# Performance work log

Hardware: AMD Instinct MI355X
Metric: run time of the kernel (lower is better)

Reference implementation:

```python
import jax, jax.numpy as jnp
import numpy as np

HIDDEN = 512
NHEADS = 8
ALPHA = 0.1
NUM_HOP = 4
MASK_VAL = -16384.0
LN_EPS = 1e-5


def setup_inputs() -> dict:
    key = jax.random.key(0)
    ks = jax.random.split(key, 10)
    B, N, H = 8, 1024, HIDDEN
    s = 1.0 / np.sqrt(H)
    x = jax.random.normal(ks[0], (B, N, H), dtype=jnp.float32)
    adj = jax.random.randint(ks[1], (B, N, N), 0, 2, dtype=jnp.int32)
    Wq = jax.random.uniform(ks[2], (H, H), jnp.float32, -s, s)
    bq = jax.random.uniform(ks[3], (H,), jnp.float32, -s, s)
    Wk = jax.random.uniform(ks[4], (H, H), jnp.float32, -s, s)
    bk = jax.random.uniform(ks[5], (H,), jnp.float32, -s, s)
    Wv = jax.random.uniform(ks[6], (H, H), jnp.float32, -s, s)
    bv = jax.random.uniform(ks[7], (H,), jnp.float32, -s, s)
    gamma = jnp.ones((H,), jnp.float32)
    beta = jnp.zeros((H,), jnp.float32)
    return {"x": x, "adj": adj, "Wq": Wq, "bq": bq, "Wk": Wk, "bk": bk,
            "Wv": Wv, "bv": bv, "gamma": gamma, "beta": beta}


def reference(x, adj, Wq, bq, Wk, bk, Wv, bv, gamma, beta):
    B, N, H = x.shape
    u = H // NHEADS
    # torch Linear: y = x @ W^T + b
    q = x @ Wq.T + bq  # [B,N,H]
    k = x @ Wk.T + bk
    v = x @ Wv.T + bv
    # split hidden into contiguous head chunks (matches per-head slicing)
    qh = q.reshape(B, N, NHEADS, u).transpose(0, 2, 1, 3)  # [B,Hd,N,u]
    kh = k.reshape(B, N, NHEADS, u).transpose(0, 2, 1, 3)
    vh = v.reshape(B, N, NHEADS, u).transpose(0, 2, 1, 3)
    scores = jnp.einsum('bhnd,bhmd->bhnm', qh, kh)  # [B,Hd,N,N]
    mask = (adj == 0)[:, None, :, :]  # broadcast over heads
    scores = jnp.where(mask, MASK_VAL, scores)
    pros = jax.nn.softmax(scores, axis=-1)
    z_init = vh
    z = z_init
    for _ in range(NUM_HOP):
        z = (1.0 - ALPHA) * jnp.einsum('bhnm,bhmd->bhnd', pros, z) + ALPHA * z_init
    h_prime = z.transpose(0, 2, 1, 3).reshape(B, N, H)  # concat heads
    y = x + h_prime
    mu = jnp.mean(y, axis=-1, keepdims=True)
    var = jnp.mean((y - mu) ** 2, axis=-1, keepdims=True)
    return (y - mu) / jnp.sqrt(var + LN_EPS) * gamma + beta
```

## Files before the change

kernel.cpp:

```cpp
#include <hip/hip_runtime.h>
#include <hip/hip_bf16.h>

#define BB 8
#define NN 1024
#define HH 512
#define NHEADS 8
#define UU 64

typedef __attribute__((ext_vector_type(8))) short short8;
typedef __attribute__((ext_vector_type(4))) float f32x4;
typedef unsigned short u16;
typedef unsigned char u8;

__device__ inline float b2f(unsigned short u) {
    union { float f; unsigned int i; } c; c.i = ((unsigned int)u) << 16; return c.f;
}
__device__ inline unsigned short f2b(float f) {
    __hip_bfloat16 h = __float2bfloat16(f);
    return *reinterpret_cast<unsigned short*>(&h);
}
__device__ inline void gl_lds16(const void* g, void* l) {
    __builtin_amdgcn_global_load_lds(
        (const __attribute__((address_space(1))) unsigned int*)g,
        (__attribute__((address_space(3))) unsigned int*)l, 16, 0, 0);
}

__global__ __launch_bounds__(256) void cvt_bf16(
    const float* __restrict__ x, const float* __restrict__ Wq,
    const float* __restrict__ Wk, const float* __restrict__ Wv,
    u16* __restrict__ xb, u16* __restrict__ Wb)
{
    const int which = blockIdx.y;
    const float* src;
    u16* dst;
    int n;
    if (which == 0) { src = x;  dst = xb;              n = BB * NN * HH; }
    else if (which == 1) { src = Wq; dst = Wb;             n = HH * HH; }
    else if (which == 2) { src = Wk; dst = Wb + HH * HH;   n = HH * HH; }
    else              { src = Wv; dst = Wb + 2 * HH * HH;  n = HH * HH; }

    const int base = (blockIdx.x * 256 + threadIdx.x) * 8;
    if (base >= n) return;
    const float4* sp = (const float4*)&src[base];
    float4 a = sp[0], b = sp[1];
    short8 o;
    o[0] = (short)f2b(a.x); o[1] = (short)f2b(a.y);
    o[2] = (short)f2b(a.z); o[3] = (short)f2b(a.w);
    o[4] = (short)f2b(b.x); o[5] = (short)f2b(b.y);
    o[6] = (short)f2b(b.z); o[7] = (short)f2b(b.w);
    *(short8*)&dst[base] = o;
}

__global__ __launch_bounds__(256) void adj_pack(
    const int* __restrict__ adj, unsigned int* __restrict__ adjp)
{
    const int wave = threadIdx.x >> 6, lane = threadIdx.x & 63;
    const int row = blockIdx.x * 4 + wave;
    const int* ar = adj + (size_t)row * NN;
    unsigned long long* out = (unsigned long long*)(adjp + (size_t)row * 32);
    #pragma unroll
    for (int it = 0; it < 16; ++it) {
        int a = ar[it * 64 + lane];
        unsigned long long m = __ballot(a != 0);
        if (lane == 0) out[it] = m;
    }
}

__global__ __launch_bounds__(256) void qkv_gemm(
    const u16* __restrict__ xb, const u16* __restrict__ Wb,
    const float* __restrict__ bq, const float* __restrict__ bk,
    const float* __restrict__ bv,
    u16* __restrict__ q, u16* __restrict__ k, u16* __restrict__ v)
{
    const int which = blockIdx.z;
    const u16* W      = Wb + which * HH * HH;
    const float* bias = which == 0 ? bq : (which == 1 ? bk : bv);
    u16* out          = which == 0 ? q  : (which == 1 ? k  : v);

    const int tid = threadIdx.x;
    const int wave = tid >> 6, lane = tid & 63;
    const int ln = lane & 15, quad = lane >> 4;
    const int wr = (wave >> 1) * 64, wc = (wave & 1) * 64;
    const int rowbase = blockIdx.x * 128, colbase = blockIdx.y * 128;

    __shared__ __align__(16) u16 As[128 * 32];
    __shared__ __align__(16) u16 Bs[128 * 32];
    __shared__ __align__(16) u16 Cs[128 * 136];

    f32x4 acc[4][4];
    #pragma unroll
    for (int ri = 0; ri < 4; ++ri)
        #pragma unroll
        for (int ci = 0; ci < 4; ++ci) acc[ri][ci] = (f32x4){0.f, 0.f, 0.f, 0.f};

    const int lr = lane >> 2;
    const int lk = (lane & 3) * 8;

    for (int kk = 0; kk < HH; kk += 32) {
        __syncthreads();
        #pragma unroll
        for (int i = 0; i < 2; ++i) {
            int r = wave * 32 + i * 16 + lr;
            gl_lds16(&xb[(size_t)(rowbase + r) * HH + kk + lk],
                     (char*)As + (wave * 32 + i * 16) * 64);
            gl_lds16(&W[(size_t)(colbase + r) * HH + kk + lk],
                     (char*)Bs + (wave * 32 + i * 16) * 64);
        }
        __syncthreads();

        short8 bfr[4];
        #pragma unroll
        for (int ci = 0; ci < 4; ++ci)
            bfr[ci] = *(const short8*)&Bs[(wc + ci * 16 + ln) * 32 + quad * 8];
        #pragma unroll
        for (int ri = 0; ri < 4; ++ri) {
            short8 af = *(const short8*)&As[(wr + ri * 16 + ln) * 32 + quad * 8];
            #pragma unroll
            for (int ci = 0; ci < 4; ++ci)
                acc[ri][ci] = __builtin_amdgcn_mfma_f32_16x16x32_bf16(af, bfr[ci], acc[ri][ci], 0, 0, 0);
        }
    }

    #pragma unroll
    for (int ci = 0; ci < 4; ++ci) {
        int col = wc + ci * 16 + ln;
        float bb = bias[colbase + col];
        #pragma unroll
        for (int ri = 0; ri < 4; ++ri) {
            #pragma unroll
            for (int r = 0; r < 4; ++r) {
                int row = wr + ri * 16 + quad * 4 + r;
                Cs[row * 136 + col] = f2b(acc[ri][ci][r] + bb);
            }
        }
    }
    __syncthreads();
    {
        int row = tid >> 1, half = tid & 1;
        int gcol0 = colbase + half * 64;
        int hh = gcol0 >> 6;
        int grow = rowbase + row;
        int bidx = grow >> 10, n = grow & 1023;
        u16* op = &out[(((size_t)(bidx * NHEADS + hh)) * NN + n) * UU];
        const u16* cp = &Cs[row * 136 + half * 64];
        #pragma unroll
        for (int j = 0; j < 8; ++j)
            *(short8*)(op + j * 8) = *(const short8*)(cp + j * 8);
    }
}

__global__ __launch_bounds__(256) void vt8(
    const u16* __restrict__ v, u8* __restrict__ v8t)
{
    const int bh = blockIdx.x;
    const int t = threadIdx.x;
    const size_t hd = (size_t)bh << 16;
    __shared__ u16 tile[64][72];

    for (int chunk = 0; chunk < 16; ++chunk) {
        const int n0 = chunk * 64;
        const int r = t >> 2, cs = t & 3;
        const u16* vp = &v[((size_t)bh * NN + n0 + r) * UU + cs * 16];
        short8 a = *(const short8*)vp;
        short8 b8 = *(const short8*)(vp + 8);
        #pragma unroll
        for (int j = 0; j < 8; ++j) {
            tile[r][cs * 16 + j] = (u16)a[j];
            tile[r][cs * 16 + 8 + j] = (u16)b8[j];
        }
        __syncthreads();
        const int c = t & 63, qt = t >> 6;
        unsigned int w[4];
        #pragma unroll
        for (int g = 0; g < 4; ++g) {
            float f0 = b2f(tile[qt * 16 + g * 4 + 0][c]);
            float f1 = b2f(tile[qt * 16 + g * 4 + 1][c]);
            float f2 = b2f(tile[qt * 16 + g * 4 + 2][c]);
            float f3 = b2f(tile[qt * 16 + g * 4 + 3][c]);
            int lo = __builtin_amdgcn_cvt_pk_fp8_f32(f0, f1, 0, false);
            w[g] = (unsigned int)__builtin_amdgcn_cvt_pk_fp8_f32(f2, f3, lo, true);
        }
        uint4 o; o.x = w[0]; o.y = w[1]; o.z = w[2]; o.w = w[3];
        *(uint4*)&v8t[hd + (size_t)c * 1024 + n0 + qt * 16] = o;
        __syncthreads();
    }
}

__global__ __launch_bounds__(256, 4) void scores_softmax(
    const u16* __restrict__ q, const u16* __restrict__ kmat,
    const unsigned int* __restrict__ adjp, u8* __restrict__ P8)
{
    const int b = blockIdx.z, h = blockIdx.y, rt = blockIdx.x;
    const int bh = b * NHEADS + h;
    const int wave = threadIdx.x >> 6, lane = threadIdx.x & 63;
    const int ln = lane & 15, quad = lane >> 4;
    const int rowbase = rt * 16;

    __shared__ float redsum[4][16];
    __shared__ float scl[16];
    __shared__ __align__(16) u16 ebuf[16 * 1040];

    const u16* qp = &q[((size_t)bh * NN + rowbase + ln) * UU + quad * 8];
    short8 a0 = *(const short8*)qp;
    short8 a1 = *(const short8*)(qp + 32);

    float rsum[4] = {0.f, 0.f, 0.f, 0.f};

    #pragma unroll
    for (int hf = 0; hf < 2; ++hf) {
        unsigned int ab[4][4];
        #pragma unroll
        for (int r = 0; r < 4; ++r) {
            int row = rowbase + quad * 4 + r;
            *(uint4*)&ab[r][0] =
                *(const uint4*)&adjp[((size_t)(b * NN + row)) * 32 + wave * 8 + hf * 4];
        }

        f32x4 accs[8];
        #pragma unroll
        for (int ct = 0; ct < 8; ++ct) {
            int col = wave * 256 + hf * 128 + ct * 16 + ln;
            const u16* kp = &kmat[((size_t)bh * NN + col) * UU + quad * 8];
            short8 b0 = *(const short8*)kp;
            short8 b1 = *(const short8*)(kp + 32);
            f32x4 acc = (f32x4){0.f, 0.f, 0.f, 0.f};
            acc = __builtin_amdgcn_mfma_f32_16x16x32_bf16(a0, b0, acc, 0, 0, 0);
            acc = __builtin_amdgcn_mfma_f32_16x16x32_bf16(a1, b1, acc, 0, 0, 0);
            accs[ct] = acc;
        }

        #pragma unroll
        for (int ct = 0; ct < 8; ++ct) {
            const int dw = ct >> 1;
            const int bitpos = (ct & 1) * 16 + ln;
            const int col = wave * 256 + hf * 128 + ct * 16 + ln;
            #pragma unroll
            for (int r = 0; r < 4; ++r) {
                unsigned int on = (ab[r][dw] >> bitpos) & 1u;
                float e = on ? __expf(accs[ct][r] - 32.0f) : 0.0f;
                rsum[r] += e;
                ebuf[(quad * 4 + r) * 1040 + col] = f2b(e);
            }
        }
    }

    #pragma unroll
    for (int r = 0; r < 4; ++r) {
        #pragma unroll
        for (int off = 8; off >= 1; off >>= 1)
            rsum[r] += __shfl_xor(rsum[r], off);
    }
    if (ln == 0) {
        #pragma unroll
        for (int r = 0; r < 4; ++r) redsum[wave][quad * 4 + r] = rsum[r];
    }
    __syncthreads();
    if (wave == 0 && ln == 0) {
        #pragma unroll
        for (int r = 0; r < 4; ++r) {
            int row16 = quad * 4 + r;
            float s = redsum[0][row16] + redsum[1][row16]
                    + redsum[2][row16] + redsum[3][row16];
            scl[row16] = 16.0f / s;
        }
    }
    __syncthreads();

    u8* Pb = P8 + ((size_t)bh << 20) + rt * 16384;
    int cc = threadIdx.x * 2;
    #pragma unroll
    for (int i = 0; i < 2; ++i, ++cc) {
        const int kc = cc >> 4, r = cc & 15;
        const float s = scl[r];
        const u16* ep = &ebuf[r * 1040 + kc * 32];
        unsigned int w[8];
        #pragma unroll
        for (int g = 0; g < 8; ++g) {
            float f0 = b2f(ep[g * 4 + 0]) * s;
            float f1 = b2f(ep[g * 4 + 1]) * s;
            float f2 = b2f(ep[g * 4 + 2]) * s;
            float f3 = b2f(ep[g * 4 + 3]) * s;
            int lo = __builtin_amdgcn_cvt_pk_fp8_f32(f0, f1, 0, false);
            w[g] = (unsigned int)__builtin_amdgcn_cvt_pk_fp8_f32(f2, f3, lo, true);
        }
        uint4 o0; o0.x = w[0]; o0.y = w[1]; o0.z = w[2]; o0.w = w[3];
        uint4 o1; o1.x = w[4]; o1.y = w[5]; o1.z = w[6]; o1.w = w[7];
        *(uint4*)(Pb + cc * 32)      = o0;
        *(uint4*)(Pb + cc * 32 + 16) = o1;
    }
}

__global__ __launch_bounds__(512) void hop(
    const u8* __restrict__ P8, const u8* __restrict__ z8in,
    const u16* __restrict__ v, u8* __restrict__ z8out,
    u16* __restrict__ zbf_out, int last)
{
    const int b = blockIdx.z, h = blockIdx.y, rt = blockIdx.x;
    const int bh = b * NHEADS + h;
    const int tid = threadIdx.x;
    const int wave = tid >> 6, lane = tid & 63;
    const int ln = lane & 15, quad = lane >> 4;
    const int wrow = rt * 128 + wave * 16;

    __shared__ __align__(16) u8 zt[64 * 1040];

    const u8* zg = z8in + ((size_t)bh << 16);
    #pragma unroll
    for (int i = 0; i < 8; ++i) {
        int c = wave * 8 + i;
        gl_lds16(zg + (size_t)c * 1024 + lane * 16, (char*)zt + c * 1040);
    }
    __syncthreads();

    f32x4 acc[4];
    #pragma unroll
    for (int ci = 0; ci < 4; ++ci) acc[ci] = (f32x4){0.f, 0.f, 0.f, 0.f};

    const u8* pt = P8 + ((size_t)bh << 20) + (size_t)(rt * 8 + wave) * 16384
                 + ln * 32 + quad * 8;
    #pragma unroll 4
    for (int kc = 0; kc < 32; ++kc) {
        long a = *(const long*)(pt + kc * 512);
        int kk = kc * 32;
        #pragma unroll
        for (int ci = 0; ci < 4; ++ci) {
            long bz = *(const long*)&zt[(ci * 16 + ln) * 1040 + kk + quad * 8];
            acc[ci] = __builtin_amdgcn_mfma_f32_16x16x32_fp8_fp8(a, bz, acc[ci], 0, 0, 0);
        }
    }

    if (last) {
        #pragma unroll
        for (int ci = 0; ci < 4; ++ci) {
            int col = ci * 16 + ln;
            #pragma unroll
            for (int r = 0; r < 4; ++r) {
                int row = wrow + quad * 4 + r;
                float vv = b2f(v[((size_t)bh * NN + row) * UU + col]);
                zbf_out[((size_t)(b * NN + row)) * HH + h * UU + col]
                    = f2b(0.05625f * acc[ci][r] + 0.1f * vv);
            }
        }
    } else {
        u8* zo = z8out + ((size_t)bh << 16);
        #pragma unroll
        for (int ci = 0; ci < 4; ++ci) {
            int col = ci * 16 + ln;
            float zv[4];
            #pragma unroll
            for (int r = 0; r < 4; ++r) {
                int row = wrow + quad * 4 + r;
                float vv = b2f(v[((size_t)bh * NN + row) * UU + col]);
                zv[r] = 0.05625f * acc[ci][r] + 0.1f * vv;
            }
            int lo = __builtin_amdgcn_cvt_pk_fp8_f32(zv[0], zv[1], 0, false);
            unsigned int dw = (unsigned int)__builtin_amdgcn_cvt_pk_fp8_f32(zv[2], zv[3], lo, true);
            *(unsigned int*)&zo[(size_t)col * 1024 + wrow + quad * 4] = dw;
        }
    }
}

__global__ __launch_bounds__(256) void resid_ln(
    const float* __restrict__ x, const u16* __restrict__ z,
    const float* __restrict__ gamma, const float* __restrict__ beta,
    float* __restrict__ out)
{
    const int r = blockIdx.x * 4 + (threadIdx.x >> 6);
    const int lane = threadIdx.x & 63;
    const size_t base = (size_t)r * HH + lane * 8;

    const float4* xp = (const float4*)&x[base];
    float4 x0 = xp[0], x1 = xp[1];
    short8 zv = *(const short8*)&z[base];
    float y[8];
    y[0] = x0.x + b2f((u16)zv[0]); y[1] = x0.y + b2f((u16)zv[1]);
    y[2] = x0.z + b2f((u16)zv[2]); y[3] = x0.w + b2f((u16)zv[3]);
    y[4] = x1.x + b2f((u16)zv[4]); y[5] = x1.y + b2f((u16)zv[5]);
    y[6] = x1.z + b2f((u16)zv[6]); y[7] = x1.w + b2f((u16)zv[7]);

    float s = 0.f, sq = 0.f;
    #pragma unroll
    for (int j = 0; j < 8; ++j) { s += y[j]; sq += y[j] * y[j]; }
    #pragma unroll
    for (int off = 32; off >= 1; off >>= 1) {
        s  += __shfl_xor(s, off);
        sq += __shfl_xor(sq, off);
    }
    const float mu = s * (1.0f / HH);
    const float var = sq * (1.0f / HH) - mu * mu;
    const float rstd = rsqrtf(var + 1e-5f);

    const float4* gp = (const float4*)&gamma[lane * 8];
    const float4* bp = (const float4*)&beta[lane * 8];
    float4 g0 = gp[0], g1 = gp[1], b0 = bp[0], b1 = bp[1];

    float4 o0, o1;
    o0.x = (y[0] - mu) * rstd * g0.x + b0.x;
    o0.y = (y[1] - mu) * rstd * g0.y + b0.y;
    o0.z = (y[2] - mu) * rstd * g0.z + b0.z;
    o0.w = (y[3] - mu) * rstd * g0.w + b0.w;
    o1.x = (y[4] - mu) * rstd * g1.x + b1.x;
    o1.y = (y[5] - mu) * rstd * g1.y + b1.y;
    o1.z = (y[6] - mu) * rstd * g1.z + b1.z;
    o1.w = (y[7] - mu) * rstd * g1.w + b1.w;
    float4* op = (float4*)&out[base];
    op[0] = o0; op[1] = o1;
}

extern "C" void kernel_launch(void* const* d_in, const int* in_sizes, int n_in,
                              void* d_out, int out_size, void* d_ws, size_t ws_size,
                              hipStream_t stream)
{
    const float* x   = (const float*)d_in[0];
    const int* adj   = (const int*)d_in[1];
    const float* Wq  = (const float*)d_in[2];
    const float* bq  = (const float*)d_in[3];
    const float* Wk  = (const float*)d_in[4];
    const float* bk  = (const float*)d_in[5];
    const float* Wv  = (const float*)d_in[6];
    const float* bv  = (const float*)d_in[7];
    const float* gamma = (const float*)d_in[8];
    const float* beta  = (const float*)d_in[9];
    float* out = (float*)d_out;

    const size_t E = (size_t)BB * NN * HH;
    u16* ws16 = (u16*)d_ws;
    u16* xb = ws16;
    u16* q  = ws16 + E;
    u16* k  = ws16 + 2 * E;
    u16* v  = ws16 + 3 * E;
    u16* za = ws16 + 4 * E;
    u16* Wb = ws16 + 5 * E;
    u8* base8 = (u8*)(ws16 + 5 * E + 786432);
    u8* P8  = base8;
    u8* z8a = base8 + ((size_t)64 << 20);
    u8* z8b = z8a + ((size_t)4 << 20);
    u8* v8t = z8b + ((size_t)4 << 20);
    unsigned int* adjp = (unsigned int*)(v8t + ((size_t)4 << 20));

    cvt_bf16<<<dim3(2048, 4), 256, 0, stream>>>(x, Wq, Wk, Wv, xb, Wb);
    adj_pack<<<dim3(2048), 256, 0, stream>>>(adj, adjp);
    qkv_gemm<<<dim3(64, 4, 3), 256, 0, stream>>>(xb, Wb, bq, bk, bv, q, k, v);
    vt8<<<dim3(64), 256, 0, stream>>>(v, v8t);
    scores_softmax<<<dim3(64, NHEADS, BB), 256, 0, stream>>>(q, k, adjp, P8);
    hop<<<dim3(8, NHEADS, BB), 512, 0, stream>>>(P8, v8t, v, z8a, za, 0);
    hop<<<dim3(8, NHEADS, BB), 512, 0, stream>>>(P8, z8a, v, z8b, za, 0);
    hop<<<dim3(8, NHEADS, BB), 512, 0, stream>>>(P8, z8b, v, z8a, za, 0);
    hop<<<dim3(8, NHEADS, BB), 512, 0, stream>>>(P8, z8a, v, z8b, za, 1);
    resid_ln<<<dim3(2048), 256, 0, stream>>>(x, za, gamma, beta, out);
}
```

Baseline: 312.1 us.

## Fuse x bf16 conversion into QKV GEMM, split vt8, restructure scores softmax

The QKV GEMM now reads fp32 x directly and converts it to bf16 while staging into padded LDS, so the separate full-activation conversion pass and its intermediate buffer go away; the weight conversion becomes a small dedicated kernel. The vt8 transpose is split across four times as many blocks to raise parallelism. scores_softmax is reorganised into 64-row tiles with K staged in LDS and a two-pass scheme: the first pass computes row sums, the second recomputes the scores and writes scaled fp8 probabilities. This drops the large per-row exp buffer but doubles the QK^T MFMA work and the exp evaluations.

```diff
diff --git a/kernel.cpp b/kernel.cpp
--- a/kernel.cpp
+++ b/kernel.cpp
@@ -25,22 +25,14 @@
         (__attribute__((address_space(3))) unsigned int*)l, 16, 0, 0);
 }
 
-__global__ __launch_bounds__(256) void cvt_bf16(
-    const float* __restrict__ x, const float* __restrict__ Wq,
-    const float* __restrict__ Wk, const float* __restrict__ Wv,
-    u16* __restrict__ xb, u16* __restrict__ Wb)
+__global__ __launch_bounds__(256) void cvt_w(
+    const float* __restrict__ Wq, const float* __restrict__ Wk,
+    const float* __restrict__ Wv, u16* __restrict__ Wb)
 {
     const int which = blockIdx.y;
-    const float* src;
-    u16* dst;
-    int n;
-    if (which == 0) { src = x;  dst = xb;              n = BB * NN * HH; }
-    else if (which == 1) { src = Wq; dst = Wb;             n = HH * HH; }
-    else if (which == 2) { src = Wk; dst = Wb + HH * HH;   n = HH * HH; }
-    else              { src = Wv; dst = Wb + 2 * HH * HH;  n = HH * HH; }
-
+    const float* src = which == 0 ? Wq : (which == 1 ? Wk : Wv);
+    u16* dst = Wb + (size_t)which * HH * HH;
     const int base = (blockIdx.x * 256 + threadIdx.x) * 8;
-    if (base >= n) return;
     const float4* sp = (const float4*)&src[base];
     float4 a = sp[0], b = sp[1];
     short8 o;
@@ -67,13 +59,13 @@
 }
 
 __global__ __launch_bounds__(256) void qkv_gemm(
-    const u16* __restrict__ xb, const u16* __restrict__ Wb,
+    const float* __restrict__ x, const u16* __restrict__ Wb,
     const float* __restrict__ bq, const float* __restrict__ bk,
     const float* __restrict__ bv,
     u16* __restrict__ q, u16* __restrict__ k, u16* __restrict__ v)
 {
     const int which = blockIdx.z;
-    const u16* W      = Wb + which * HH * HH;
+    const u16* W      = Wb + (size_t)which * HH * HH;
     const float* bias = which == 0 ? bq : (which == 1 ? bk : bv);
     u16* out          = which == 0 ? q  : (which == 1 ? k  : v);
 
@@ -83,7 +75,7 @@
     const int wr = (wave >> 1) * 64, wc = (wave & 1) * 64;
     const int rowbase = blockIdx.x * 128, colbase = blockIdx.y * 128;
 
-    __shared__ __align__(16) u16 As[128 * 32];
+    __shared__ __align__(16) u16 As[128 * 40];
     __shared__ __align__(16) u16 Bs[128 * 32];
     __shared__ __align__(16) u16 Cs[128 * 136];
 
@@ -94,16 +86,22 @@
         for (int ci = 0; ci < 4; ++ci) acc[ri][ci] = (f32x4){0.f, 0.f, 0.f, 0.f};
 
     const int lr = lane >> 2;
-    const int lk = (lane & 3) * 8;
+    const int sg = lane & 3;
 
     for (int kk = 0; kk < HH; kk += 32) {
         __syncthreads();
         #pragma unroll
         for (int i = 0; i < 2; ++i) {
             int r = wave * 32 + i * 16 + lr;
-            gl_lds16(&xb[(size_t)(rowbase + r) * HH + kk + lk],
-                     (char*)As + (wave * 32 + i * 16) * 64);
-            gl_lds16(&W[(size_t)(colbase + r) * HH + kk + lk],
+            const float* xp = &x[(size_t)(rowbase + r) * HH + kk + sg * 8];
+            float4 f0 = *(const float4*)xp, f1 = *(const float4*)(xp + 4);
+            short8 o;
+            o[0] = (short)f2b(f0.x); o[1] = (short)f2b(f0.y);
+            o[2] = (short)f2b(f0.z); o[3] = (short)f2b(f0.w);
+            o[4] = (short)f2b(f1.x); o[5] = (short)f2b(f1.y);
+            o[6] = (short)f2b(f1.z); o[7] = (short)f2b(f1.w);
+            *(short8*)&As[r * 40 + sg * 8] = o;
+            gl_lds16(&W[(size_t)(colbase + r) * HH + kk + sg * 8],
                      (char*)Bs + (wave * 32 + i * 16) * 64);
         }
         __syncthreads();
@@ -114,7 +112,7 @@
             bfr[ci] = *(const short8*)&Bs[(wc + ci * 16 + ln) * 32 + quad * 8];
         #pragma unroll
         for (int ri = 0; ri < 4; ++ri) {
-            short8 af = *(const short8*)&As[(wr + ri * 16 + ln) * 32 + quad * 8];
+            short8 af = *(const short8*)&As[(wr + ri * 16 + ln) * 40 + quad * 8];
             #pragma unroll
             for (int ci = 0; ci < 4; ++ci)
                 acc[ri][ci] = __builtin_amdgcn_mfma_f32_16x16x32_bf16(af, bfr[ci], acc[ri][ci], 0, 0, 0);
@@ -152,12 +150,12 @@
 __global__ __launch_bounds__(256) void vt8(
     const u16* __restrict__ v, u8* __restrict__ v8t)
 {
-    const int bh = blockIdx.x;
+    const int bh = blockIdx.x >> 2, part = blockIdx.x & 3;
     const int t = threadIdx.x;
     const size_t hd = (size_t)bh << 16;
     __shared__ u16 tile[64][72];
 
-    for (int chunk = 0; chunk < 16; ++chunk) {
+    for (int chunk = part * 4; chunk < part * 4 + 4; ++chunk) {
         const int n0 = chunk * 64;
         const int r = t >> 2, cs = t & 3;
         const u16* vp = &v[((size_t)bh * NN + n0 + r) * UU + cs * 16];
@@ -186,107 +184,105 @@
     }
 }
 
-__global__ __launch_bounds__(256, 4) void scores_softmax(
+__global__ __launch_bounds__(256) void scores_softmax(
     const u16* __restrict__ q, const u16* __restrict__ kmat,
     const unsigned int* __restrict__ adjp, u8* __restrict__ P8)
 {
     const int b = blockIdx.z, h = blockIdx.y, rt = blockIdx.x;
     const int bh = b * NHEADS + h;
-    const int wave = threadIdx.x >> 6, lane = threadIdx.x & 63;
+    const int tid = threadIdx.x;
+    const int wave = tid >> 6, lane = tid & 63;
     const int ln = lane & 15, quad = lane >> 4;
-    const int rowbase = rt * 16;
-
-    __shared__ float redsum[4][16];
-    __shared__ float scl[16];
-    __shared__ __align__(16) u16 ebuf[16 * 1040];
-
-    const u16* qp = &q[((size_t)bh * NN + rowbase + ln) * UU + quad * 8];
+    const int wrow = rt * 64 + wave * 16;
+
+    __shared__ __align__(16) u16 ks[128 * 72];
+    __shared__ __align__(16) u16 eb[64 * 136];
+
+    const u16* qp = &q[((size_t)bh * NN + wrow + ln) * UU + quad * 8];
     short8 a0 = *(const short8*)qp;
     short8 a1 = *(const short8*)(qp + 32);
 
     float rsum[4] = {0.f, 0.f, 0.f, 0.f};
-
-    #pragma unroll
-    for (int hf = 0; hf < 2; ++hf) {
-        unsigned int ab[4][4];
-        #pragma unroll
-        for (int r = 0; r < 4; ++r) {
-            int row = rowbase + quad * 4 + r;
-            *(uint4*)&ab[r][0] =
-                *(const uint4*)&adjp[((size_t)(b * NN + row)) * 32 + wave * 8 + hf * 4];
-        }
-
-        f32x4 accs[8];
-        #pragma unroll
-        for (int ct = 0; ct < 8; ++ct) {
-            int col = wave * 256 + hf * 128 + ct * 16 + ln;
-            const u16* kp = &kmat[((size_t)bh * NN + col) * UU + quad * 8];
-            short8 b0 = *(const short8*)kp;
-            short8 b1 = *(const short8*)(kp + 32);
-            f32x4 acc = (f32x4){0.f, 0.f, 0.f, 0.f};
-            acc = __builtin_amdgcn_mfma_f32_16x16x32_bf16(a0, b0, acc, 0, 0, 0);
-            acc = __builtin_amdgcn_mfma_f32_16x16x32_bf16(a1, b1, acc, 0, 0, 0);
-            accs[ct] = acc;
-        }
-
-        #pragma unroll
-        for (int ct = 0; ct < 8; ++ct) {
-            const int dw = ct >> 1;
-            const int bitpos = (ct & 1) * 16 + ln;
-            const int col = wave * 256 + hf * 128 + ct * 16 + ln;
+    float scl[4];
+
+    const int srow = tid >> 3;
+    const int sseg = tid & 7;
+
+    for (int pass = 0; pass < 2; ++pass) {
+        for (int cc = 0; cc < 8; ++cc) {
+            __syncthreads();
+            #pragma unroll
+            for (int j = 0; j < 4; ++j) {
+                int kr = j * 32 + srow;
+                uint4 kv = *(const uint4*)&kmat[((size_t)bh * NN + cc * 128 + kr) * UU + sseg * 8];
+                *(uint4*)&ks[kr * 72 + sseg * 8] = kv;
+            }
+            __syncthreads();
+
+            unsigned int ab[4][4];
             #pragma unroll
             for (int r = 0; r < 4; ++r) {
-                unsigned int on = (ab[r][dw] >> bitpos) & 1u;
-                float e = on ? __expf(accs[ct][r] - 32.0f) : 0.0f;
-                rsum[r] += e;
-                ebuf[(quad * 4 + r) * 1040 + col] = f2b(e);
-            }
-        }
-    }
-
-    #pragma unroll
-    for (int r = 0; r < 4; ++r) {
-        #pragma unroll
-        for (int off = 8; off >= 1; off >>= 1)
-            rsum[r] += __shfl_xor(rsum[r], off);
-    }
-    if (ln == 0) {
-        #pragma unroll
-        for (int r = 0; r < 4; ++r) redsum[wave][quad * 4 + r] = rsum[r];
-    }
-    __syncthreads();
-    if (wave == 0 && ln == 0) {
-        #pragma unroll
-        for (int r = 0; r < 4; ++r) {
-            int row16 = quad * 4 + r;
-            float s = redsum[0][row16] + redsum[1][row16]
-                    + redsum[2][row16] + redsum[3][row16];
-            scl[row16] = 16.0f / s;
-        }
-    }
-    __syncthreads();
-
-    u8* Pb = P8 + ((size_t)bh << 20) + rt * 16384;
-    int cc = threadIdx.x * 2;
-    #pragma unroll
-    for (int i = 0; i < 2; ++i, ++cc) {
-        const int kc = cc >> 4, r = cc & 15;
-        const float s = scl[r];
-        const u16* ep = &ebuf[r * 1040 + kc * 32];
-        unsigned int w[8];
-        #pragma unroll
-        for (int g = 0; g < 8; ++g) {
-            float f0 = b2f(ep[g * 4 + 0]) * s;
-            float f1 = b2f(ep[g * 4 + 1]) * s;
-            float f2 = b2f(ep[g * 4 + 2]) * s;
-            float f3 = b2f(ep[g * 4 + 3]) * s;
-            int lo = __builtin_amdgcn_cvt_pk_fp8_f32(f0, f1, 0, false);
-            w[g] = (unsigned int)__builtin_amdgcn_cvt_pk_fp8_f32(f2, f3, lo, true);
-        }
-        uint4 o0; o0.x = w[0]; o0.y = w[1]; o0.z = w[2]; o0.w = w[3];
-        uint4 o1; o1.x = w[4]; o1.y = w[5]; o1.z = w[6]; o1.w = w[7];
-        *(uint4*)(Pb + cc * 32)      = o0;
-        *(uint4*)(Pb + cc * 32 + 16) = o1;
+                int row = wrow + quad * 4 + r;
+                *(uint4*)&ab[r][0] =
+                    *(const uint4*)&adjp[((size_t)(b * NN + row)) * 32 + cc * 4];
+            }
+
+            #pragma unroll
+            for (int ct = 0; ct < 8; ++ct) {
+                const u16* kp = &ks[(ct * 16 + ln) * 72 + quad * 8];
+                short8 b0 = *(const short8*)kp;
+                short8 b1 = *(const short8*)(kp + 32);
+                f32x4 acc = (f32x4){0.f, 0.f, 0.f, 0.f};
+                acc = __builtin_amdgcn_mfma_f32_16x16x32_bf16(a0, b0, acc, 0, 0, 0);
+                acc = __builtin_amdgcn_mfma_f32_16x16x32_bf16(a1, b1, acc, 0, 0, 0);
+                const int dw = ct >> 1;
+                const int bitpos = (ct & 1) * 16 + ln;
+                #pragma unroll
+                for (int r = 0; r < 4; ++r) {
+                    unsigned int on = (ab[r][dw] >> bitpos) & 1u;
+                    float e = on ? __expf(acc[r] - 32.0f) : 0.0f;
+                    if (pass == 0) rsum[r] += e;
+                    else eb[(wave * 16 + quad * 4 + r) * 136 + ct * 16 + ln] = f2b(e * scl[r]);
+                }
+            }
+
+            if (pass == 1) {
+                const int kcp = lane >> 4, r16 = lane & 15;
+                const u16* ep = &eb[(wave * 16 + r16) * 136 + kcp * 32];
+                unsigned int w[8];
+                #pragma unroll
+                for (int g2 = 0; g2 < 4; ++g2) {
+                    short8 ev = *(const short8*)(ep + g2 * 8);
+                    float f0 = b2f((u16)ev[0]);
+                    float f1 = b2f((u16)ev[1]);
+                    float f2 = b2f((u16)ev[2]);
+                    float f3 = b2f((u16)ev[3]);
+                    int lo = __builtin_amdgcn_cvt_pk_fp8_f32(f0, f1, 0, false);
+                    w[g2 * 2] = (unsigned int)__builtin_amdgcn_cvt_pk_fp8_f32(f2, f3, lo, true);
+                    f0 = b2f((u16)ev[4]);
+                    f1 = b2f((u16)ev[5]);
+                    f2 = b2f((u16)ev[6]);
+                    f3 = b2f((u16)ev[7]);
+                    lo = __builtin_amdgcn_cvt_pk_fp8_f32(f0, f1, 0, false);
+                    w[g2 * 2 + 1] = (unsigned int)__builtin_amdgcn_cvt_pk_fp8_f32(f2, f3, lo, true);
+                }
+                u8* op = P8 + ((size_t)bh << 20) + (size_t)(rt * 4 + wave) * 16384
+                       + (cc * 4 + kcp) * 512 + r16 * 32;
+                uint4 o0; o0.x = w[0]; o0.y = w[1]; o0.z = w[2]; o0.w = w[3];
+                uint4 o1; o1.x = w[4]; o1.y = w[5]; o1.z = w[6]; o1.w = w[7];
+                *(uint4*)op = o0;
+                *(uint4*)(op + 16) = o1;
+            }
+        }
+        if (pass == 0) {
+            #pragma unroll
+            for (int r = 0; r < 4; ++r) {
+                #pragma unroll
+                for (int off = 8; off >= 1; off >>= 1)
+                    rsum[r] += __shfl_xor(rsum[r], off);
+                scl[r] = 16.0f / rsum[r];
+            }
+        }
     }
 }
 
@@ -425,7 +421,6 @@
 
     const size_t E = (size_t)BB * NN * HH;
     u16* ws16 = (u16*)d_ws;
-    u16* xb = ws16;
     u16* q  = ws16 + E;
     u16* k  = ws16 + 2 * E;
     u16* v  = ws16 + 3 * E;
@@ -438,11 +433,11 @@
     u8* v8t = z8b + ((size_t)4 << 20);
     unsigned int* adjp = (unsigned int*)(v8t + ((size_t)4 << 20));
 
-    cvt_bf16<<<dim3(2048, 4), 256, 0, stream>>>(x, Wq, Wk, Wv, xb, Wb);
+    cvt_w<<<dim3(128, 3), 256, 0, stream>>>(Wq, Wk, Wv, Wb);
     adj_pack<<<dim3(2048), 256, 0, stream>>>(adj, adjp);
-    qkv_gemm<<<dim3(64, 4, 3), 256, 0, stream>>>(xb, Wb, bq, bk, bv, q, k, v);
-    vt8<<<dim3(64), 256, 0, stream>>>(v, v8t);
-    scores_softmax<<<dim3(64, NHEADS, BB), 256, 0, stream>>>(q, k, adjp, P8);
+    qkv_gemm<<<dim3(64, 4, 3), 256, 0, stream>>>(x, Wb, bq, bk, bv, q, k, v);
+    vt8<<<dim3(256), 256, 0, stream>>>(v, v8t);
+    scores_softmax<<<dim3(16, NHEADS, BB), 256, 0, stream>>>(q, k, adjp, P8);
     hop<<<dim3(8, NHEADS, BB), 512, 0, stream>>>(P8, v8t, v, z8a, za, 0);
     hop<<<dim3(8, NHEADS, BB), 512, 0, stream>>>(P8, z8a, v, z8b, za, 0);
     hop<<<dim3(8, NHEADS, BB), 512, 0, stream>>>(P8, z8b, v, z8a, za, 0);
```

Result: faster. 287.9 us (-7.7%).
